# Performance work log

Hardware: AMD Instinct MI355X
Metric: run time of the kernel (lower is better)

Reference implementation:

```python
import jax, jax.numpy as jnp
import numpy as np

B, S, D, H = 4, 2048, 1024, 16
DK = D // H
DFF = 4 * D
EPS = 1e-5


def layernorm(x, g, b):
    mu = jnp.mean(x, axis=-1, keepdims=True)
    var = jnp.var(x, axis=-1, keepdims=True)
    return (x - mu) * jax.lax.rsqrt(var + EPS) * g + b


def setup_inputs() -> dict:
    key = jax.random.key(0)
    ks = jax.random.split(key, 16)
    s_d = 1.0 / np.sqrt(D)
    s_f = 1.0 / np.sqrt(DFF)
    return {
        "x": jax.random.normal(ks[0], (B, S, D), jnp.float32),
        # attention projections (qkv_bias=False); weights stored [in, out]
        "wq": jax.random.normal(ks[1], (D, D), jnp.float32) * s_d,
        "wk": jax.random.normal(ks[2], (D, D), jnp.float32) * s_d,
        "wv": jax.random.normal(ks[3], (D, D), jnp.float32) * s_d,
        "wo": jax.random.normal(ks[4], (D, D), jnp.float32) * s_d,
        "bo": jax.random.normal(ks[5], (D,), jnp.float32) * s_d,
        # feedforward
        "w1": jax.random.normal(ks[6], (D, DFF), jnp.float32) * s_d,
        "b1": jax.random.normal(ks[7], (DFF,), jnp.float32) * s_d,
        "w2": jax.random.normal(ks[8], (DFF, D), jnp.float32) * s_f,
        "b2": jax.random.normal(ks[9], (D,), jnp.float32) * s_f,
        # layernorms
        "g1": jnp.ones((D,), jnp.float32),
        "be1": jnp.zeros((D,), jnp.float32),
        "g2": jnp.ones((D,), jnp.float32),
        "be2": jnp.zeros((D,), jnp.float32),
    }


def reference(x, wq, wk, wv, wo, bo, w1, b1, w2, b2, g1, be1, g2, be2):
    # dropout is identity at inference
    shortcut = x
    h = layernorm(x, g1, be1)
    # multi-head causal attention (naive, materializes [B,H,S,S])
    q = (h @ wq).reshape(B, S, H, DK).transpose(0, 2, 1, 3)
    k = (h @ wk).reshape(B, S, H, DK).transpose(0, 2, 1, 3)
    v = (h @ wv).reshape(B, S, H, DK).transpose(0, 2, 1, 3)
    scores = jnp.einsum("bhqd,bhkd->bhqk", q, k)
    causal = jnp.triu(jnp.ones((S, S), bool), k=1)
    scores = jnp.where(causal, -jnp.inf, scores)
    attn = jax.nn.softmax(scores / np.sqrt(DK), axis=-1)
    out = jnp.einsum("bhqk,bhkd->bhqd", attn, v)
    out = out.transpose(0, 2, 1, 3).reshape(B, S, D)
    x = out @ wo + bo + shortcut
    shortcut = x
    h = layernorm(x, g2, be2)
    h = jax.nn.gelu(h @ w1 + b1, approximate=False) @ w2 + b2
    return h + shortcut
```

## Files before the change

kernel.cpp:

```cpp
#include <hip/hip_runtime.h>


typedef unsigned short ushort;
typedef __attribute__((ext_vector_type(8))) short bf16x8;
typedef __attribute__((ext_vector_type(4))) float f32x4;
typedef __attribute__((ext_vector_type(4))) unsigned short ushort4v;

#define B_ 4
#define S_ 2048
#define D_ 1024
#define H_ 16
#define DK_ 64
#define DFF_ 4096

__device__ __forceinline__ float b2f(ushort u){
  union { unsigned int i; float f; } x; x.i = ((unsigned int)u) << 16; return x.f;
}
__device__ __forceinline__ ushort f2b(float f){
  union { float f; unsigned int i; } x; x.f = f;
  return (ushort)((x.i + 0x7fffu + ((x.i >> 16) & 1u)) >> 16);
}

__device__ __forceinline__ f32x4 mfma16(bf16x8 a, bf16x8 b, f32x4 c){
  return __builtin_amdgcn_mfma_f32_16x16x32_bf16(a, b, c, 0, 0, 0);
}

__global__ void transpose_f32_bf16(const float* __restrict__ in,
                                   ushort* __restrict__ out, int K, int N){
  __shared__ ushort t[32][33];
  int k0 = blockIdx.y * 32, n0 = blockIdx.x * 32;
  for (int i = threadIdx.y; i < 32; i += 8)
    t[i][threadIdx.x] = f2b(in[(size_t)(k0 + i) * N + n0 + threadIdx.x]);
  __syncthreads();
  for (int i = threadIdx.y; i < 32; i += 8)
    out[(size_t)(n0 + i) * K + k0 + threadIdx.x] = t[threadIdx.x][i];
}

__global__ __launch_bounds__(256) void ln_f32(
    const float* __restrict__ x, const float* __restrict__ g,
    const float* __restrict__ be, ushort* __restrict__ out){
  int row = blockIdx.x; int t = threadIdx.x;
  const float* xr = x + (size_t)row * D_;
  float4 v = *(const float4*)(xr + t * 4);
  float s = v.x + v.y + v.z + v.w;
  float q = v.x*v.x + v.y*v.y + v.z*v.z + v.w*v.w;
  for (int off = 32; off; off >>= 1){
    s += __shfl_down(s, off);
    q += __shfl_down(q, off);
  }
  __shared__ float ss[4], sq[4];
  int wave = t >> 6, lane = t & 63;
  if (lane == 0){ ss[wave] = s; sq[wave] = q; }
  __syncthreads();
  float ts = ss[0] + ss[1] + ss[2] + ss[3];
  float tq = sq[0] + sq[1] + sq[2] + sq[3];
  float mu  = ts * (1.0f / D_);
  float var = tq * (1.0f / D_) - mu * mu;
  float rstd = rsqrtf(var + 1e-5f);
  float4 gv = *(const float4*)(g  + t * 4);
  float4 bv = *(const float4*)(be + t * 4);
  ushort4v o;
  o[0] = f2b((v.x - mu) * rstd * gv.x + bv.x);
  o[1] = f2b((v.y - mu) * rstd * gv.y + bv.y);
  o[2] = f2b((v.z - mu) * rstd * gv.z + bv.z);
  o[3] = f2b((v.w - mu) * rstd * gv.w + bv.w);
  *(ushort4v*)(out + (size_t)row * D_ + t * 4) = o;
}

template<int MODE>
__global__ __launch_bounds__(256) void gemm_bf16(
    const ushort* __restrict__ A, const ushort* __restrict__ Bt,
    void* __restrict__ Cv, const float* __restrict__ bias,
    const float* __restrict__ resf, int M, int N, int K)
{
  __shared__ ushort As[128 * 32];
  __shared__ ushort Bs[128 * 32];
  int m0 = blockIdx.y * 128, n0 = blockIdx.x * 128;
  int t = threadIdx.x;
  int sr = t >> 2, sc = (t & 3) << 3;
  int wv = t >> 6, lane = t & 63;
  int wr = wv >> 1, wc = wv & 1;
  int lg = lane >> 4, lr = lane & 15;

  f32x4 acc[4][4];
  for (int i = 0; i < 4; i++)
    for (int j = 0; j < 4; j++) acc[i][j] = (f32x4){0.f, 0.f, 0.f, 0.f};

  int nkt = K >> 5;
  for (int kt = 0; kt < nkt; ++kt){
    __syncthreads();
    const ushort* Ag = A  + (size_t)(m0 + sr) * K + (kt << 5) + sc;
    const ushort* Bg = Bt + (size_t)(n0 + sr) * K + (kt << 5) + sc;
    *(bf16x8*)(As + sr * 32 + sc)        = *(const bf16x8*)(Ag);
    *(bf16x8*)(As + (sr + 64) * 32 + sc) = *(const bf16x8*)(Ag + (size_t)64 * K);
    *(bf16x8*)(Bs + sr * 32 + sc)        = *(const bf16x8*)(Bg);
    *(bf16x8*)(Bs + (sr + 64) * 32 + sc) = *(const bf16x8*)(Bg + (size_t)64 * K);
    __syncthreads();
    bf16x8 af[4], bfr[4];
    for (int i = 0; i < 4; i++)
      af[i]  = *(const bf16x8*)(As + (wr * 64 + i * 16 + lr) * 32 + lg * 8);
    for (int j = 0; j < 4; j++)
      bfr[j] = *(const bf16x8*)(Bs + (wc * 64 + j * 16 + lr) * 32 + lg * 8);
    for (int i = 0; i < 4; i++)
      for (int j = 0; j < 4; j++)
        acc[i][j] = mfma16(af[i], bfr[j], acc[i][j]);
  }

  for (int i = 0; i < 4; i++){
    int mb = m0 + wr * 64 + i * 16 + lg * 4;
    for (int j = 0; j < 4; j++){
      int ng = n0 + wc * 64 + j * 16 + lr;
      for (int r = 0; r < 4; r++){
        int mg = mb + r;
        float vacc = acc[i][j][r];
        if constexpr (MODE == 0){
          int b = mg >> 11, si = mg & 2047;
          int hh = ng >> 6, dk = ng & 63;
          ((ushort*)Cv)[((((size_t)b * H_ + hh) * S_ + si) << 6) + dk] = f2b(vacc);
        } else if constexpr (MODE == 1){
          int b = mg >> 11, si = mg & 2047;
          int hh = ng >> 6, dk = ng & 63;
          ((ushort*)Cv)[((((size_t)b * H_ + hh) * DK_ + dk) << 11) + si] = f2b(vacc);
        } else if constexpr (MODE == 2){
          size_t idx = (size_t)mg * N + ng;
          ((float*)Cv)[idx] = vacc + bias[ng] + resf[idx];
        } else {
          size_t idx = (size_t)mg * N + ng;
          float xv = vacc + bias[ng];
          float gel = xv * 0.5f * (1.0f + erff(xv * 0.70710678118f));
          ((ushort*)Cv)[idx] = f2b(gel);
        }
      }
    }
  }
}

__global__ __launch_bounds__(256) void attn_fwd(
    const ushort* __restrict__ qg, const ushort* __restrict__ kg,
    const ushort* __restrict__ vg, ushort* __restrict__ outp)
{
  int h = blockIdx.y, b = blockIdx.z;
  int wave = threadIdx.x >> 6, lane = threadIdx.x & 63;
  int lg = lane >> 4, lr = lane & 15;
  int qbase = blockIdx.x * 64 + wave * 16;
  const ushort* qp = qg + (((size_t)b * H_ + h) * S_) * DK_;
  const ushort* kp = kg + (((size_t)b * H_ + h) * S_) * DK_;
  const ushort* vp = vg + (((size_t)b * H_ + h) * DK_) * S_;
  __shared__ ushort plds[4][16][32];

  bf16x8 aq0 = *(const bf16x8*)(qp + (size_t)(qbase + lr) * DK_ + lg * 8);
  bf16x8 aq1 = *(const bf16x8*)(qp + (size_t)(qbase + lr) * DK_ + 32 + lg * 8);

  float m[4], l[4];
  f32x4 oacc[4];
  for (int r = 0; r < 4; r++){ m[r] = -3.0e38f; l[r] = 0.f; }
  for (int c = 0; c < 4; c++) oacc[c] = (f32x4){0.f, 0.f, 0.f, 0.f};

  int nkt = (qbase + 15) / 32 + 1;
  for (int kt = 0; kt < nkt; ++kt){
    int kb = kt * 32;
    f32x4 s[2];
    for (int kk = 0; kk < 2; kk++){
      bf16x8 bk0 = *(const bf16x8*)(kp + (size_t)(kb + kk * 16 + lr) * DK_ + lg * 8);
      bf16x8 bk1 = *(const bf16x8*)(kp + (size_t)(kb + kk * 16 + lr) * DK_ + 32 + lg * 8);
      f32x4 z = (f32x4){0.f, 0.f, 0.f, 0.f};
      s[kk] = mfma16(aq0, bk0, z);
      s[kk] = mfma16(aq1, bk1, s[kk]);
    }
    bool domask = (kb + 31) > qbase;
    for (int kk = 0; kk < 2; kk++)
      for (int r = 0; r < 4; r++){
        float sv = s[kk][r] * 0.125f;
        if (domask){
          int qgl = qbase + lg * 4 + r;
          int kgl = kb + kk * 16 + lr;
          if (kgl > qgl) sv = -1.0e30f;
        }
        s[kk][r] = sv;
      }
    float p0[4], p1[4], alpha[4];
    for (int r = 0; r < 4; r++){
      float rm = fmaxf(s[0][r], s[1][r]);
      for (int off = 1; off < 16; off <<= 1) rm = fmaxf(rm, __shfl_xor(rm, off));
      float mnew = fmaxf(m[r], rm);
      alpha[r] = expf(m[r] - mnew);
      p0[r] = expf(s[0][r] - mnew);
      p1[r] = expf(s[1][r] - mnew);
      float rs = p0[r] + p1[r];
      for (int off = 1; off < 16; off <<= 1) rs += __shfl_xor(rs, off);
      l[r] = l[r] * alpha[r] + rs;
      m[r] = mnew;
    }
    for (int c = 0; c < 4; c++)
      for (int r = 0; r < 4; r++) oacc[c][r] *= alpha[r];
    for (int r = 0; r < 4; r++){
      plds[wave][lg * 4 + r][lr]      = f2b(p0[r]);
      plds[wave][lg * 4 + r][16 + lr] = f2b(p1[r]);
    }
    bf16x8 pa = *(const bf16x8*)(&plds[wave][lr][lg * 8]);
    for (int c = 0; c < 4; c++){
      bf16x8 bv = *(const bf16x8*)(vp + (size_t)(c * 16 + lr) * S_ + kb + lg * 8);
      oacc[c] = mfma16(pa, bv, oacc[c]);
    }
  }
  for (int c = 0; c < 4; c++)
    for (int r = 0; r < 4; r++){
      size_t row = (size_t)b * S_ + qbase + lg * 4 + r;
      outp[row * D_ + h * DK_ + c * 16 + lr] = f2b(oacc[c][r] / l[r]);
    }
}

extern "C" void kernel_launch(void* const* d_in, const int* in_sizes, int n_in,
                              void* d_out, int out_size, void* d_ws, size_t ws_size,
                              hipStream_t stream)
{
  const float* x   = (const float*)d_in[0];
  const float* wq  = (const float*)d_in[1];
  const float* wk  = (const float*)d_in[2];
  const float* wv  = (const float*)d_in[3];
  const float* wo  = (const float*)d_in[4];
  const float* bo  = (const float*)d_in[5];
  const float* w1  = (const float*)d_in[6];
  const float* b1  = (const float*)d_in[7];
  const float* w2  = (const float*)d_in[8];
  const float* b2  = (const float*)d_in[9];
  const float* g1  = (const float*)d_in[10];
  const float* be1 = (const float*)d_in[11];
  const float* g2  = (const float*)d_in[12];
  const float* be2 = (const float*)d_in[13];

  char* ws = (char*)d_ws;
  const size_t MB = 1ull << 20;
  ushort* wqT  = (ushort*)(ws + 0 * MB);
  ushort* wkT  = (ushort*)(ws + 2 * MB);
  ushort* wvT  = (ushort*)(ws + 4 * MB);
  ushort* woT  = (ushort*)(ws + 6 * MB);
  ushort* w1T  = (ushort*)(ws + 8 * MB);
  ushort* w2T  = (ushort*)(ws + 16 * MB);
  ushort* hbuf = (ushort*)(ws + 24 * MB);
  ushort* qbuf = (ushort*)(ws + 40 * MB);
  ushort* kbuf = (ushort*)(ws + 56 * MB);
  ushort* vbuf = (ushort*)(ws + 72 * MB);
  float*  x2f  = (float*)(ws + 88 * MB);

  dim3 tb(32, 8);
  transpose_f32_bf16<<<dim3(32, 32), tb, 0, stream>>>(wq, wqT, 1024, 1024);
  transpose_f32_bf16<<<dim3(32, 32), tb, 0, stream>>>(wk, wkT, 1024, 1024);
  transpose_f32_bf16<<<dim3(32, 32), tb, 0, stream>>>(wv, wvT, 1024, 1024);
  transpose_f32_bf16<<<dim3(32, 32), tb, 0, stream>>>(wo, woT, 1024, 1024);
  transpose_f32_bf16<<<dim3(128, 32), tb, 0, stream>>>(w1, w1T, 1024, 4096);
  transpose_f32_bf16<<<dim3(32, 128), tb, 0, stream>>>(w2, w2T, 4096, 1024);

  ln_f32<<<8192, 256, 0, stream>>>(x, g1, be1, hbuf);

  gemm_bf16<0><<<dim3(8, 64), 256, 0, stream>>>(hbuf, wqT, qbuf, nullptr, nullptr, 8192, 1024, 1024);
  gemm_bf16<0><<<dim3(8, 64), 256, 0, stream>>>(hbuf, wkT, kbuf, nullptr, nullptr, 8192, 1024, 1024);
  gemm_bf16<1><<<dim3(8, 64), 256, 0, stream>>>(hbuf, wvT, vbuf, nullptr, nullptr, 8192, 1024, 1024);

  attn_fwd<<<dim3(32, 16, 4), 256, 0, stream>>>(qbuf, kbuf, vbuf, hbuf);

  gemm_bf16<2><<<dim3(8, 64), 256, 0, stream>>>(hbuf, woT, x2f, bo, x, 8192, 1024, 1024);

  ln_f32<<<8192, 256, 0, stream>>>(x2f, g2, be2, kbuf);

  for (int c = 0; c < 4; ++c){
    const ushort* h2c = kbuf + (size_t)c * 2048 * 1024;
    float* outc = (float*)d_out + (size_t)c * 2048 * 1024;
    const float* x2c = x2f + (size_t)c * 2048 * 1024;
    gemm_bf16<3><<<dim3(32, 16), 256, 0, stream>>>(h2c, w1T, vbuf, b1, nullptr, 2048, 4096, 1024);
    gemm_bf16<2><<<dim3(8, 16), 256, 0, stream>>>(vbuf, w2T, outc, b2, x2c, 2048, 1024, 4096);
  }
}
```

Baseline: 1.748 ms.

## Fuse QKV projections into one GEMM and stage tiles with direct global-to-LDS loads

Concatenates the transposed Q, K and V weights and runs a single 8192x3072 GEMM whose epilogue routes each output column to the right head-split buffer, replacing three launches. The GEMM tile staging now uses global_load_lds builtins so global data is written straight into shared memory without passing through registers. Mode numbering is renumbered to match. The direct-to-LDS loads change the LDS layout per wave, which must match the fragment reads, and the per-element branch in the QKV epilogue adds some overhead.

```diff
diff --git a/kernel.cpp b/kernel.cpp
--- a/kernel.cpp
+++ b/kernel.cpp
@@ -23,6 +23,12 @@
 
 __device__ __forceinline__ f32x4 mfma16(bf16x8 a, bf16x8 b, f32x4 c){
   return __builtin_amdgcn_mfma_f32_16x16x32_bf16(a, b, c, 0, 0, 0);
+}
+
+__device__ __forceinline__ void gload16(const ushort* g, ushort* l){
+  __builtin_amdgcn_global_load_lds(
+      (const __attribute__((address_space(1))) void*)g,
+      (__attribute__((address_space(3))) void*)l, 16, 0, 0);
 }
 
 __global__ void transpose_f32_bf16(const float* __restrict__ in,
@@ -70,17 +76,18 @@
 template<int MODE>
 __global__ __launch_bounds__(256) void gemm_bf16(
     const ushort* __restrict__ A, const ushort* __restrict__ Bt,
-    void* __restrict__ Cv, const float* __restrict__ bias,
-    const float* __restrict__ resf, int M, int N, int K)
+    void* __restrict__ C0, void* __restrict__ C1, void* __restrict__ C2,
+    const float* __restrict__ bias, const float* __restrict__ resf,
+    int M, int N, int K)
 {
   __shared__ ushort As[128 * 32];
   __shared__ ushort Bs[128 * 32];
   int m0 = blockIdx.y * 128, n0 = blockIdx.x * 128;
   int t = threadIdx.x;
-  int sr = t >> 2, sc = (t & 3) << 3;
   int wv = t >> 6, lane = t & 63;
   int wr = wv >> 1, wc = wv & 1;
   int lg = lane >> 4, lr = lane & 15;
+  int lrow = lane >> 2, lcol = (lane & 3) << 3;
 
   f32x4 acc[4][4];
   for (int i = 0; i < 4; i++)
@@ -89,12 +96,14 @@
   int nkt = K >> 5;
   for (int kt = 0; kt < nkt; ++kt){
     __syncthreads();
-    const ushort* Ag = A  + (size_t)(m0 + sr) * K + (kt << 5) + sc;
-    const ushort* Bg = Bt + (size_t)(n0 + sr) * K + (kt << 5) + sc;
-    *(bf16x8*)(As + sr * 32 + sc)        = *(const bf16x8*)(Ag);
-    *(bf16x8*)(As + (sr + 64) * 32 + sc) = *(const bf16x8*)(Ag + (size_t)64 * K);
-    *(bf16x8*)(Bs + sr * 32 + sc)        = *(const bf16x8*)(Bg);
-    *(bf16x8*)(Bs + (sr + 64) * 32 + sc) = *(const bf16x8*)(Bg + (size_t)64 * K);
+    {
+      const ushort* Ag = A  + (size_t)(m0 + wv * 16 + lrow) * K + (kt << 5) + lcol;
+      const ushort* Bg = Bt + (size_t)(n0 + wv * 16 + lrow) * K + (kt << 5) + lcol;
+      gload16(Ag,                    As + wv * 512);
+      gload16(Ag + (size_t)64 * K,   As + 2048 + wv * 512);
+      gload16(Bg,                    Bs + wv * 512);
+      gload16(Bg + (size_t)64 * K,   Bs + 2048 + wv * 512);
+    }
     __syncthreads();
     bf16x8 af[4], bfr[4];
     for (int i = 0; i < 4; i++)
@@ -115,20 +124,22 @@
         float vacc = acc[i][j][r];
         if constexpr (MODE == 0){
           int b = mg >> 11, si = mg & 2047;
-          int hh = ng >> 6, dk = ng & 63;
-          ((ushort*)Cv)[((((size_t)b * H_ + hh) * S_ + si) << 6) + dk] = f2b(vacc);
+          int which = ng >> 10;
+          int hh = (ng >> 6) & 15, dk = ng & 63;
+          if (which == 0)
+            ((ushort*)C0)[((((size_t)b * H_ + hh) * S_ + si) << 6) + dk] = f2b(vacc);
+          else if (which == 1)
+            ((ushort*)C1)[((((size_t)b * H_ + hh) * S_ + si) << 6) + dk] = f2b(vacc);
+          else
+            ((ushort*)C2)[((((size_t)b * H_ + hh) * DK_ + dk) << 11) + si] = f2b(vacc);
         } else if constexpr (MODE == 1){
-          int b = mg >> 11, si = mg & 2047;
-          int hh = ng >> 6, dk = ng & 63;
-          ((ushort*)Cv)[((((size_t)b * H_ + hh) * DK_ + dk) << 11) + si] = f2b(vacc);
-        } else if constexpr (MODE == 2){
           size_t idx = (size_t)mg * N + ng;
-          ((float*)Cv)[idx] = vacc + bias[ng] + resf[idx];
+          ((float*)C0)[idx] = vacc + bias[ng] + resf[idx];
         } else {
           size_t idx = (size_t)mg * N + ng;
           float xv = vacc + bias[ng];
           float gel = xv * 0.5f * (1.0f + erff(xv * 0.70710678118f));
-          ((ushort*)Cv)[idx] = f2b(gel);
+          ((ushort*)C0)[idx] = f2b(gel);
         }
       }
     }
@@ -231,9 +242,7 @@
 
   char* ws = (char*)d_ws;
   const size_t MB = 1ull << 20;
-  ushort* wqT  = (ushort*)(ws + 0 * MB);
-  ushort* wkT  = (ushort*)(ws + 2 * MB);
-  ushort* wvT  = (ushort*)(ws + 4 * MB);
+  ushort* wqkvT = (ushort*)(ws + 0 * MB);
   ushort* woT  = (ushort*)(ws + 6 * MB);
   ushort* w1T  = (ushort*)(ws + 8 * MB);
   ushort* w2T  = (ushort*)(ws + 16 * MB);
@@ -244,22 +253,22 @@
   float*  x2f  = (float*)(ws + 88 * MB);
 
   dim3 tb(32, 8);
-  transpose_f32_bf16<<<dim3(32, 32), tb, 0, stream>>>(wq, wqT, 1024, 1024);
-  transpose_f32_bf16<<<dim3(32, 32), tb, 0, stream>>>(wk, wkT, 1024, 1024);
-  transpose_f32_bf16<<<dim3(32, 32), tb, 0, stream>>>(wv, wvT, 1024, 1024);
+  transpose_f32_bf16<<<dim3(32, 32), tb, 0, stream>>>(wq, wqkvT, 1024, 1024);
+  transpose_f32_bf16<<<dim3(32, 32), tb, 0, stream>>>(wk, wqkvT + (1024ull*1024), 1024, 1024);
+  transpose_f32_bf16<<<dim3(32, 32), tb, 0, stream>>>(wv, wqkvT + (2048ull*1024), 1024, 1024);
   transpose_f32_bf16<<<dim3(32, 32), tb, 0, stream>>>(wo, woT, 1024, 1024);
   transpose_f32_bf16<<<dim3(128, 32), tb, 0, stream>>>(w1, w1T, 1024, 4096);
   transpose_f32_bf16<<<dim3(32, 128), tb, 0, stream>>>(w2, w2T, 4096, 1024);
 
   ln_f32<<<8192, 256, 0, stream>>>(x, g1, be1, hbuf);
 
-  gemm_bf16<0><<<dim3(8, 64), 256, 0, stream>>>(hbuf, wqT, qbuf, nullptr, nullptr, 8192, 1024, 1024);
-  gemm_bf16<0><<<dim3(8, 64), 256, 0, stream>>>(hbuf, wkT, kbuf, nullptr, nullptr, 8192, 1024, 1024);
-  gemm_bf16<1><<<dim3(8, 64), 256, 0, stream>>>(hbuf, wvT, vbuf, nullptr, nullptr, 8192, 1024, 1024);
+  gemm_bf16<0><<<dim3(24, 64), 256, 0, stream>>>(hbuf, wqkvT, qbuf, kbuf, vbuf,
+                                                 nullptr, nullptr, 8192, 3072, 1024);
 
   attn_fwd<<<dim3(32, 16, 4), 256, 0, stream>>>(qbuf, kbuf, vbuf, hbuf);
 
-  gemm_bf16<2><<<dim3(8, 64), 256, 0, stream>>>(hbuf, woT, x2f, bo, x, 8192, 1024, 1024);
+  gemm_bf16<1><<<dim3(8, 64), 256, 0, stream>>>(hbuf, woT, x2f, nullptr, nullptr,
+                                                bo, x, 8192, 1024, 1024);
 
   ln_f32<<<8192, 256, 0, stream>>>(x2f, g2, be2, kbuf);
 
@@ -267,7 +276,9 @@
     const ushort* h2c = kbuf + (size_t)c * 2048 * 1024;
     float* outc = (float*)d_out + (size_t)c * 2048 * 1024;
     const float* x2c = x2f + (size_t)c * 2048 * 1024;
-    gemm_bf16<3><<<dim3(32, 16), 256, 0, stream>>>(h2c, w1T, vbuf, b1, nullptr, 2048, 4096, 1024);
-    gemm_bf16<2><<<dim3(8, 16), 256, 0, stream>>>(vbuf, w2T, outc, b2, x2c, 2048, 1024, 4096);
-  }
-}
+    gemm_bf16<2><<<dim3(32, 16), 256, 0, stream>>>(h2c, w1T, vbuf, nullptr, nullptr,
+                                                   b1, nullptr, 2048, 4096, 1024);
+    gemm_bf16<1><<<dim3(8, 16), 256, 0, stream>>>(vbuf, w2T, outc, nullptr, nullptr,
+                                                  b2, x2c, 2048, 1024, 4096);
+  }
+}
```

Result: no change. 1.731 ms (-1.0%).
